# Kernel optimization log

Hardware: AMD Instinct MI355X
Metric: run time of the kernel (lower is better)

Reference implementation:

```python
import jax, jax.numpy as jnp
import numpy as np

N_NODES = 50000
N_EDGES = 800000
IN_CH = 64
OC = 16  # out_channels


def setup_inputs() -> dict:
    key = jax.random.key(0)
    ks = jax.random.split(key, 16)
    x = jax.random.normal(ks[0], (N_NODES, IN_CH), dtype=jnp.float32)
    edge_index = jax.random.randint(ks[1], (2, N_EDGES), 0, N_NODES, dtype=jnp.int64)

    def lin(k, fan_in, fan_out):
        s = 1.0 / np.sqrt(fan_in)
        return jax.random.uniform(k, (fan_in, fan_out), jnp.float32, -s, s)

    d1, d2 = 16 * OC, 8 * OC  # 256, 128
    return {
        "x": x,
        "W1_rel": lin(ks[2], IN_CH, d1), "b1": jnp.zeros((d1,), jnp.float32), "W1_root": lin(ks[3], IN_CH, d1),
        "W2_rel": lin(ks[4], d1, d2), "b2": jnp.zeros((d2,), jnp.float32), "W2_root": lin(ks[5], d1, d2),
        "Wmu_rel": lin(ks[6], d2, OC), "bmu": jnp.zeros((OC,), jnp.float32), "Wmu_root": lin(ks[7], d2, OC),
        "Wls_rel": lin(ks[8], d2, OC), "bls": jnp.zeros((OC,), jnp.float32), "Wls_root": lin(ks[9], d2, OC),
        "edge_index": edge_index,
    }


def _graph_conv(x, src, dst, deg_inv, W_rel, b, W_root):
    # PyG GraphConv(aggr='mean'): out = lin_rel(mean_{j in N(i)} x_j) + lin_root(x_i)
    msg_sum = jax.ops.segment_sum(x[src], dst, num_segments=x.shape[0])  # [N, d]
    agg = msg_sum * deg_inv[:, None]
    return agg @ W_rel + b + x @ W_root


def reference(x, W1_rel, b1, W1_root, W2_rel, b2, W2_root,
              Wmu_rel, bmu, Wmu_root, Wls_rel, bls, Wls_root, edge_index):
    src, dst = edge_index[0], edge_index[1]
    deg = jax.ops.segment_sum(jnp.ones_like(dst, dtype=x.dtype), dst, num_segments=x.shape[0])
    deg_inv = jnp.where(deg > 0, 1.0 / jnp.maximum(deg, 1.0), 0.0)

    h = jax.nn.relu(_graph_conv(x, src, dst, deg_inv, W1_rel, b1, W1_root))
    h = jax.nn.relu(_graph_conv(h, src, dst, deg_inv, W2_rel, b2, W2_root))
    mu = _graph_conv(h, src, dst, deg_inv, Wmu_rel, bmu, Wmu_root)
    logstd = _graph_conv(h, src, dst, deg_inv, Wls_rel, bls, Wls_root)
    return (mu, logstd)
```

## Files before the change

kernel.cpp:

```cpp
#include <hip/hip_runtime.h>
#include <hip/hip_fp8.h>

#define N_NODES 50000
#define N_EDGES 800000
#define NBUCK 196
#define PBLK 391
#define CAP 5120

typedef unsigned short ushort_t;
typedef unsigned char uchar_t;
typedef short short8 __attribute__((ext_vector_type(8)));
typedef float floatx4 __attribute__((ext_vector_type(4)));

__device__ __forceinline__ float bf2f(ushort_t u) {
    unsigned v = ((unsigned)u) << 16;
    return __builtin_bit_cast(float, v);
}
__device__ __forceinline__ ushort_t f2bf(float f) {
    unsigned u = __builtin_bit_cast(unsigned, f);
    unsigned r = (u + 0x7FFFu + ((u >> 16) & 1u)) >> 16;
    return (ushort_t)r;
}
__device__ __forceinline__ uchar_t f2fp8(float f) {
    __hip_fp8_e4m3 t(f);
    return (uchar_t)t.__x;
}
__device__ __forceinline__ float fp82f(uchar_t u) {
    __hip_fp8_e4m3 t;
    t.__x = (__hip_fp8_storage_t)u;
    return (float)t;
}
__device__ __forceinline__ float4 ld4(const float* p) { return *(const float4*)p; }

__global__ __launch_bounds__(256) void prep_kernel(
    const float* __restrict__ x,
    const float* __restrict__ W1_rel, const float* __restrict__ W1_root,
    const float* __restrict__ W2_rel, const float* __restrict__ W2_root,
    const float* __restrict__ Wmu_rel, const float* __restrict__ Wls_rel,
    const float* __restrict__ Wmu_root, const float* __restrict__ Wls_root,
    ushort_t* __restrict__ xb, uchar_t* __restrict__ xq,
    ushort_t* __restrict__ B1t, ushort_t* __restrict__ B2t, ushort_t* __restrict__ B3t,
    int* __restrict__ bcursor) {
    int idx = blockIdx.x * blockDim.x + threadIdx.x;
    if (idx < 400000) {
        int n = idx >> 3, c = (idx & 7) * 8;
        float4 v0 = ld4(x + (size_t)n * 64 + c);
        float4 v1 = ld4(x + (size_t)n * 64 + c + 4);
        float vv[8] = {v0.x, v0.y, v0.z, v0.w, v1.x, v1.y, v1.z, v1.w};
        short8 o;
        unsigned q0 = 0, q1 = 0;
        #pragma unroll
        for (int i = 0; i < 4; ++i) {
            o[i] = f2bf(vv[i]);
            o[4 + i] = f2bf(vv[4 + i]);
            q0 |= ((unsigned)f2fp8(vv[i])) << (8 * i);
            q1 |= ((unsigned)f2fp8(vv[4 + i])) << (8 * i);
        }
        *(short8*)(xb + (size_t)n * 64 + c) = o;
        uint2 q = {q0, q1};
        *(uint2*)(xq + (size_t)n * 64 + c) = q;
    } else if (idx < 506496) {
        int j = idx - 400000;
        if (j < 32768) {
            int n = j >> 7, k = j & 127;
            float v = (k < 64) ? W1_rel[k * 256 + n] : W1_root[(k - 64) * 256 + n];
            B1t[j] = f2bf(v);
        } else if (j < 98304) {
            int jj = j - 32768;
            int n = jj >> 8, k = jj & 255;
            float v = (n < 128) ? W2_rel[k * 128 + n] : W2_root[k * 128 + (n - 128)];
            B2t[jj] = f2bf(v);
        } else {
            int jj = j - 98304;
            int n = jj >> 7, k = jj & 127;
            const float* W = (n < 16) ? Wmu_rel : (n < 32) ? Wls_rel : (n < 48) ? Wmu_root : Wls_root;
            B3t[jj] = f2bf(W[k * 16 + (n & 15)]);
        }
    } else if (idx < 506496 + NBUCK) {
        int b = idx - 506496;
        bcursor[b] = b * CAP;
    }
}

__global__ __launch_bounds__(256) void partition_kernel(
    const int* __restrict__ src, const int* __restrict__ dst,
    int* __restrict__ bcursor, unsigned* __restrict__ pairbuf) {
    __shared__ int h[NBUCK];
    __shared__ int cur[NBUCK];
    const int tid = threadIdx.x;
    for (int i = tid; i < NBUCK; i += 256) h[i] = 0;
    __syncthreads();
    const int base = blockIdx.x * 2048;
    int d[8];
    #pragma unroll
    for (int j = 0; j < 8; ++j) {
        int e = base + j * 256 + tid;
        if (e < N_EDGES) { d[j] = dst[e]; atomicAdd(&h[d[j] >> 8], 1); }
        else d[j] = -1;
    }
    __syncthreads();
    for (int i = tid; i < NBUCK; i += 256) {
        int c = h[i];
        cur[i] = c ? atomicAdd(&bcursor[i], c) : 0;
    }
    __syncthreads();
    #pragma unroll
    for (int j = 0; j < 8; ++j) {
        int e = base + j * 256 + tid;
        if (e < N_EDGES) {
            int dd = d[j];
            int slot = atomicAdd(&cur[dd >> 8], 1);
            pairbuf[slot] = (unsigned)src[e] | ((unsigned)(dd & 255) << 16);
        }
    }
}

__global__ __launch_bounds__(256) void fill_bucket_kernel(
    const unsigned* __restrict__ pairbuf, const int* __restrict__ bcursor,
    int* __restrict__ row_beg, int* __restrict__ row_end,
    float* __restrict__ dinv, ushort_t* __restrict__ eidx) {
    __shared__ int h[256];
    __shared__ int sm[256];
    __shared__ int cur[256];
    const int b = blockIdx.x, tid = threadIdx.x;
    const int beg = b * CAP, end = bcursor[b];
    h[tid] = 0;
    __syncthreads();
    for (int i = beg + tid; i < end; i += 256)
        atomicAdd(&h[pairbuf[i] >> 16], 1);
    __syncthreads();
    int c = h[tid];
    sm[tid] = c;
    __syncthreads();
    #pragma unroll
    for (int off = 1; off < 256; off <<= 1) {
        int t = (tid >= off) ? sm[tid - off] : 0;
        __syncthreads();
        sm[tid] += t;
        __syncthreads();
    }
    int exc = beg + sm[tid] - c;
    int node = b * 256 + tid;
    if (node < N_NODES) {
        row_beg[node] = exc;
        row_end[node] = exc + c;
        dinv[node] = c > 0 ? 1.0f / (float)c : 0.0f;
    }
    cur[tid] = exc;
    __syncthreads();
    for (int i = beg + tid; i < end; i += 256) {
        unsigned v = pairbuf[i];
        int slot = atomicAdd(&cur[v >> 16], 1);
        eidx[slot] = (ushort_t)(v & 0xFFFFu);
    }
}

__global__ __launch_bounds__(256) void g1gemm12(
    const ushort_t* __restrict__ xb, const uchar_t* __restrict__ xq,
    const int* __restrict__ row_beg, const int* __restrict__ row_end,
    const ushort_t* __restrict__ eidx, const float* __restrict__ dinv,
    const ushort_t* __restrict__ B1t, const float* __restrict__ b1,
    const ushort_t* __restrict__ B2t,
    uchar_t* __restrict__ t2, ushort_t* __restrict__ r2) {
    constexpr int K1 = 128, K2 = 256;
    constexpr int AKP = 72;
    constexpr int HKP = 264;
    constexpr int BKP = 264;
    __shared__ ushort_t As[64 * AKP];
    __shared__ ushort_t Hs[64 * HKP];
    __shared__ ushort_t Bs[64 * BKP];
    const int tid = threadIdx.x;
    const int rowbase = blockIdx.x * 64;

    {
        const int nl = tid >> 2, lane = tid & 3;
        const int node = rowbase + nl;
        int beg = 0, end = 0;
        float d = 0.0f;
        if (node < N_NODES) { beg = row_beg[node]; end = row_end[node]; d = dinv[node]; }
        float a0[16] = {}, a1[16] = {};
        int j = beg;
        for (; j + 1 < end; j += 2) {
            uint4 v0 = *(const uint4*)(xq + (size_t)eidx[j] * 64 + lane * 16);
            uint4 v1 = *(const uint4*)(xq + (size_t)eidx[j + 1] * 64 + lane * 16);
            #pragma unroll
            for (int i = 0; i < 4; ++i) {
                a0[i]      += fp82f((uchar_t)(v0.x >> (8 * i)));
                a0[4 + i]  += fp82f((uchar_t)(v0.y >> (8 * i)));
                a0[8 + i]  += fp82f((uchar_t)(v0.z >> (8 * i)));
                a0[12 + i] += fp82f((uchar_t)(v0.w >> (8 * i)));
                a1[i]      += fp82f((uchar_t)(v1.x >> (8 * i)));
                a1[4 + i]  += fp82f((uchar_t)(v1.y >> (8 * i)));
                a1[8 + i]  += fp82f((uchar_t)(v1.z >> (8 * i)));
                a1[12 + i] += fp82f((uchar_t)(v1.w >> (8 * i)));
            }
        }
        if (j < end) {
            uint4 v0 = *(const uint4*)(xq + (size_t)eidx[j] * 64 + lane * 16);
            #pragma unroll
            for (int i = 0; i < 4; ++i) {
                a0[i]      += fp82f((uchar_t)(v0.x >> (8 * i)));
                a0[4 + i]  += fp82f((uchar_t)(v0.y >> (8 * i)));
                a0[8 + i]  += fp82f((uchar_t)(v0.z >> (8 * i)));
                a0[12 + i] += fp82f((uchar_t)(v0.w >> (8 * i)));
            }
        }
        short8 o0, o1;
        #pragma unroll
        for (int i = 0; i < 8; ++i) {
            o0[i] = f2bf((a0[i] + a1[i]) * d);
            o1[i] = f2bf((a0[8 + i] + a1[8 + i]) * d);
        }
        *(short8*)(As + nl * AKP + lane * 16) = o0;
        *(short8*)(As + nl * AKP + lane * 16 + 8) = o1;
    }
    __syncthreads();

    const int w = tid >> 6, lane64 = tid & 63;
    const int ln = lane64 & 15, quad = lane64 >> 4;
    const int rwl = w * 16 + ln;
    int r = rowbase + rwl;
    if (r > N_NODES - 1) r = N_NODES - 1;

    short8 a[4];
    a[0] = *(const short8*)(As + rwl * AKP + quad * 8);
    a[1] = *(const short8*)(As + rwl * AKP + 32 + quad * 8);
    a[2] = *(const short8*)(xb + (size_t)r * 64 + quad * 8);
    a[3] = *(const short8*)(xb + (size_t)r * 64 + 32 + quad * 8);
    for (int ny = 0; ny < 4; ++ny) {
        __syncthreads();
        for (int i = tid; i < 64 * 16; i += 256) {
            int row = i >> 4, off = (i & 15) * 8;
            *(short8*)(Bs + row * BKP + off) = *(const short8*)(B1t + (size_t)(ny * 64 + row) * K1 + off);
        }
        __syncthreads();
        floatx4 acc[4] = {};
        #pragma unroll
        for (int f = 0; f < 4; ++f) {
            const ushort_t* bp = Bs + (f * 16 + ln) * BKP + quad * 8;
            #pragma unroll
            for (int s = 0; s < 4; ++s) {
                short8 b = *(const short8*)(bp + s * 32);
                acc[f] = __builtin_amdgcn_mfma_f32_16x16x32_bf16(a[s], b, acc[f], 0, 0, 0);
            }
        }
        #pragma unroll
        for (int f = 0; f < 4; ++f) {
            int n = ny * 64 + f * 16 + ln;
            float bias = b1[n];
            #pragma unroll
            for (int g = 0; g < 4; ++g) {
                int rr = w * 16 + quad * 4 + g;
                Hs[rr * HKP + n] = f2bf(fmaxf(acc[f][g] + bias, 0.0f));
            }
        }
    }
    __syncthreads();

    short8 a2[8];
    #pragma unroll
    for (int s = 0; s < 8; ++s)
        a2[s] = *(const short8*)(Hs + rwl * HKP + s * 32 + quad * 8);
    for (int ny = 0; ny < 4; ++ny) {
        __syncthreads();
        for (int i = tid; i < 64 * 32; i += 256) {
            int row = i >> 5, off = (i & 31) * 8;
            *(short8*)(Bs + row * BKP + off) = *(const short8*)(B2t + (size_t)(ny * 64 + row) * K2 + off);
        }
        __syncthreads();
        floatx4 acc[4] = {};
        #pragma unroll
        for (int f = 0; f < 4; ++f) {
            const ushort_t* bp = Bs + (f * 16 + ln) * BKP + quad * 8;
            #pragma unroll
            for (int s = 0; s < 8; ++s) {
                short8 b = *(const short8*)(bp + s * 32);
                acc[f] = __builtin_amdgcn_mfma_f32_16x16x32_bf16(a2[s], b, acc[f], 0, 0, 0);
            }
        }
        #pragma unroll
        for (int f = 0; f < 4; ++f) {
            int n = ny * 64 + f * 16 + ln;
            #pragma unroll
            for (int g = 0; g < 4; ++g) {
                int rr = rowbase + w * 16 + quad * 4 + g;
                if (rr >= N_NODES) continue;
                float v = acc[f][g];
                if (n < 128) t2[(size_t)rr * 128 + n] = f2fp8(v);
                else r2[(size_t)rr * 128 + (n - 128)] = f2bf(v);
            }
        }
    }
}

__global__ __launch_bounds__(256) void g2g3_kernel(
    const uchar_t* __restrict__ t2, const ushort_t* __restrict__ r2,
    const int* __restrict__ row_beg, const int* __restrict__ row_end,
    const ushort_t* __restrict__ eidx, const float* __restrict__ dinv,
    const float* __restrict__ b2, const ushort_t* __restrict__ B3t,
    ushort_t* __restrict__ tml, float* __restrict__ rml) {
    constexpr int KP = 136;
    __shared__ ushort_t As[16 * KP];
    const int tid = threadIdx.x;
    const int nb = blockIdx.x * 16;
    {
        const int nl = tid >> 4, lane = tid & 15;
        const int node = nb + nl;
        const int beg = row_beg[node], end = row_end[node];
        float a0[8] = {}, a1[8] = {}, a2[8] = {}, a3[8] = {};
        int j = beg;
        for (; j + 3 < end; j += 4) {
            uint2 v0 = *(const uint2*)(t2 + (size_t)eidx[j] * 128 + lane * 8);
            uint2 v1 = *(const uint2*)(t2 + (size_t)eidx[j + 1] * 128 + lane * 8);
            uint2 v2 = *(const uint2*)(t2 + (size_t)eidx[j + 2] * 128 + lane * 8);
            uint2 v3 = *(const uint2*)(t2 + (size_t)eidx[j + 3] * 128 + lane * 8);
            #pragma unroll
            for (int i = 0; i < 4; ++i) {
                a0[i]     += fp82f((uchar_t)(v0.x >> (8 * i)));
                a0[4 + i] += fp82f((uchar_t)(v0.y >> (8 * i)));
                a1[i]     += fp82f((uchar_t)(v1.x >> (8 * i)));
                a1[4 + i] += fp82f((uchar_t)(v1.y >> (8 * i)));
                a2[i]     += fp82f((uchar_t)(v2.x >> (8 * i)));
                a2[4 + i] += fp82f((uchar_t)(v2.y >> (8 * i)));
                a3[i]     += fp82f((uchar_t)(v3.x >> (8 * i)));
                a3[4 + i] += fp82f((uchar_t)(v3.y >> (8 * i)));
            }
        }
        for (; j < end; ++j) {
            uint2 v0 = *(const uint2*)(t2 + (size_t)eidx[j] * 128 + lane * 8);
            #pragma unroll
            for (int i = 0; i < 4; ++i) {
                a0[i]     += fp82f((uchar_t)(v0.x >> (8 * i)));
                a0[4 + i] += fp82f((uchar_t)(v0.y >> (8 * i)));
            }
        }
        float d = dinv[node];
        short8 rv = *(const short8*)(r2 + (size_t)node * 128 + lane * 8);
        float4 ba = ld4(b2 + lane * 8), bb = ld4(b2 + lane * 8 + 4);
        float bc[8] = {ba.x, ba.y, ba.z, ba.w, bb.x, bb.y, bb.z, bb.w};
        short8 o;
        #pragma unroll
        for (int i = 0; i < 8; ++i)
            o[i] = f2bf(fmaxf(((a0[i] + a1[i]) + (a2[i] + a3[i])) * d + bf2f((ushort_t)rv[i]) + bc[i], 0.0f));
        *(short8*)(As + nl * KP + lane * 8) = o;
    }
    __syncthreads();
    const int w = tid >> 6, lane64 = tid & 63;
    const int ln = lane64 & 15, quad = lane64 >> 4;
    short8 a[4];
    #pragma unroll
    for (int s = 0; s < 4; ++s)
        a[s] = *(const short8*)(As + ln * KP + s * 32 + quad * 8);
    floatx4 acc = {};
    const ushort_t* bp = B3t + (size_t)(w * 16 + ln) * 128 + quad * 8;
    #pragma unroll
    for (int s = 0; s < 4; ++s) {
        short8 b = *(const short8*)(bp + s * 32);
        acc = __builtin_amdgcn_mfma_f32_16x16x32_bf16(a[s], b, acc, 0, 0, 0);
    }
    const int r0 = nb + quad * 4;
    const int ncol = w * 16 + ln;
    #pragma unroll
    for (int g = 0; g < 4; ++g) {
        int rr = r0 + g;
        float v = acc[g];
        if (ncol < 32) tml[(size_t)rr * 32 + ncol] = f2bf(v);
        else rml[(size_t)rr * 32 + (ncol - 32)] = v;
    }
}

__global__ __launch_bounds__(256) void gather3_kernel(
    const ushort_t* __restrict__ tml, const float* __restrict__ rml,
    const int* __restrict__ row_beg, const int* __restrict__ row_end,
    const ushort_t* __restrict__ eidx, const float* __restrict__ dinv,
    const float* __restrict__ bmu, const float* __restrict__ bls,
    float* __restrict__ out) {
    const int lane = threadIdx.x & 3;
    const int nl = threadIdx.x >> 2;
    const int n = blockIdx.x * 64 + nl;
    if (n >= N_NODES) return;
    const int beg = row_beg[n], end = row_end[n];
    float a0[8] = {}, a1[8] = {}, a2[8] = {}, a3[8] = {};
    int j = beg;
    for (; j + 3 < end; j += 4) {
        short8 v0 = *(const short8*)(tml + (size_t)eidx[j] * 32 + lane * 8);
        short8 v1 = *(const short8*)(tml + (size_t)eidx[j + 1] * 32 + lane * 8);
        short8 v2 = *(const short8*)(tml + (size_t)eidx[j + 2] * 32 + lane * 8);
        short8 v3 = *(const short8*)(tml + (size_t)eidx[j + 3] * 32 + lane * 8);
        #pragma unroll
        for (int i = 0; i < 8; ++i) {
            a0[i] += bf2f((ushort_t)v0[i]); a1[i] += bf2f((ushort_t)v1[i]);
            a2[i] += bf2f((ushort_t)v2[i]); a3[i] += bf2f((ushort_t)v3[i]);
        }
    }
    for (; j < end; ++j) {
        short8 v0 = *(const short8*)(tml + (size_t)eidx[j] * 32 + lane * 8);
        #pragma unroll
        for (int i = 0; i < 8; ++i) a0[i] += bf2f((ushort_t)v0[i]);
    }
    float d = dinv[n];
    const float* bias = (lane < 2) ? (bmu + lane * 8) : (bls + (lane - 2) * 8);
    float4 ra = ld4(rml + (size_t)n * 32 + lane * 8);
    float4 rb = ld4(rml + (size_t)n * 32 + lane * 8 + 4);
    float4 ba = ld4(bias);
    float4 bb = ld4(bias + 4);
    float rr[8] = {ra.x, ra.y, ra.z, ra.w, rb.x, rb.y, rb.z, rb.w};
    float bc[8] = {ba.x, ba.y, ba.z, ba.w, bb.x, bb.y, bb.z, bb.w};
    float res[8];
    #pragma unroll
    for (int i = 0; i < 8; ++i) res[i] = ((a0[i] + a1[i]) + (a2[i] + a3[i])) * d + rr[i] + bc[i];
    float* base = (lane < 2) ? (out + (size_t)n * 16 + lane * 8)
                             : (out + 800000u + (size_t)n * 16 + (lane - 2) * 8);
    *(float4*)(base) = make_float4(res[0], res[1], res[2], res[3]);
    *(float4*)(base + 4) = make_float4(res[4], res[5], res[6], res[7]);
}

extern "C" void kernel_launch(void* const* d_in, const int* in_sizes, int n_in,
                              void* d_out, int out_size, void* d_ws, size_t ws_size,
                              hipStream_t stream) {
    const float* x       = (const float*)d_in[0];
    const float* W1_rel  = (const float*)d_in[1];
    const float* b1      = (const float*)d_in[2];
    const float* W1_root = (const float*)d_in[3];
    const float* W2_rel  = (const float*)d_in[4];
    const float* b2      = (const float*)d_in[5];
    const float* W2_root = (const float*)d_in[6];
    const float* Wmu_rel = (const float*)d_in[7];
    const float* bmu     = (const float*)d_in[8];
    const float* Wmu_root= (const float*)d_in[9];
    const float* Wls_rel = (const float*)d_in[10];
    const float* bls     = (const float*)d_in[11];
    const float* Wls_root= (const float*)d_in[12];
    const int*   ei      = (const int*)d_in[13];
    const int* src = ei;
    const int* dst = ei + N_EDGES;

    int*      bcursor = (int*)d_ws;
    int*      row_beg = bcursor + 256;
    int*      row_end = row_beg + 50048;
    unsigned* pairbuf = (unsigned*)(row_end + 50048);
    ushort_t* eidx    = (ushort_t*)(pairbuf + 1003520);
    float*    dinv    = (float*)(eidx + 1003520);
    ushort_t* xb   = (ushort_t*)(dinv + 50000);
    uchar_t*  xq   = (uchar_t*)(xb + 3200000);
    uchar_t*  t2   = xq + 3200000;
    ushort_t* r2   = (ushort_t*)(t2 + 6400000);
    ushort_t* tml  = r2 + 6400000;
    ushort_t* B1t  = tml + 1600000;
    ushort_t* B2t  = B1t + 32768;
    ushort_t* B3t  = B2t + 65536;
    float* rml     = (float*)(B3t + 8192);
    float* out     = (float*)d_out;

    prep_kernel<<<1980, 256, 0, stream>>>(x, W1_rel, W1_root, W2_rel, W2_root,
                                          Wmu_rel, Wls_rel, Wmu_root, Wls_root,
                                          xb, xq, B1t, B2t, B3t, bcursor);
    partition_kernel<<<PBLK, 256, 0, stream>>>(src, dst, bcursor, pairbuf);
    fill_bucket_kernel<<<NBUCK, 256, 0, stream>>>(pairbuf, bcursor, row_beg, row_end, dinv, eidx);

    g1gemm12<<<782, 256, 0, stream>>>(xb, xq, row_beg, row_end, eidx, dinv,
                                      B1t, b1, B2t, t2, r2);

    g2g3_kernel<<<3125, 256, 0, stream>>>(t2, r2, row_beg, row_end, eidx, dinv, b2, B3t, tml, rml);

    gather3_kernel<<<782, 256, 0, stream>>>(tml, rml, row_beg, row_end, eidx, dinv, bmu, bls, out);
}
```

Baseline: 220.6 us.

## Read GEMM weights directly from global memory and drop the shared B tile

Removes the shared-memory B staging buffer in the fused gather+GEMM kernel, so the MFMA loops load weight fragments straight from global memory (L2/L1-resident) with no block barriers per tile. Cutting LDS use and adding a launch-bounds occupancy hint of 3 blocks aims for higher occupancy. The edge gather loop is also unrolled to four neighbours per iteration for more memory-level parallelism. The risk is more global and cache traffic for the weights, plus register pressure from the occupancy cap.

Measured after the change: 265.1 us. +20.2%, slower.

```diff
diff --git a/kernel.cpp b/kernel.cpp
--- a/kernel.cpp
+++ b/kernel.cpp
@@ -31,6 +31,16 @@
     return (float)t;
 }
 __device__ __forceinline__ float4 ld4(const float* p) { return *(const float4*)p; }
+
+__device__ __forceinline__ void acc16(float* a, uint4 v) {
+    unsigned ws[4] = {v.x, v.y, v.z, v.w};
+    #pragma unroll
+    for (int wi = 0; wi < 4; ++wi) {
+        #pragma unroll
+        for (int i = 0; i < 4; ++i)
+            a[wi * 4 + i] += fp82f((uchar_t)(ws[wi] >> (8 * i)));
+    }
+}
 
 __global__ __launch_bounds__(256) void prep_kernel(
     const float* __restrict__ x,
@@ -155,7 +165,7 @@
     }
 }
 
-__global__ __launch_bounds__(256) void g1gemm12(
+__global__ __launch_bounds__(256, 3) void g1gemm12(
     const ushort_t* __restrict__ xb, const uchar_t* __restrict__ xq,
     const int* __restrict__ row_beg, const int* __restrict__ row_end,
     const ushort_t* __restrict__ eidx, const float* __restrict__ dinv,
@@ -165,10 +175,8 @@
     constexpr int K1 = 128, K2 = 256;
     constexpr int AKP = 72;
     constexpr int HKP = 264;
-    constexpr int BKP = 264;
     __shared__ ushort_t As[64 * AKP];
     __shared__ ushort_t Hs[64 * HKP];
-    __shared__ ushort_t Bs[64 * BKP];
     const int tid = threadIdx.x;
     const int rowbase = blockIdx.x * 64;
 
@@ -180,30 +188,16 @@
         if (node < N_NODES) { beg = row_beg[node]; end = row_end[node]; d = dinv[node]; }
         float a0[16] = {}, a1[16] = {};
         int j = beg;
-        for (; j + 1 < end; j += 2) {
+        for (; j + 3 < end; j += 4) {
             uint4 v0 = *(const uint4*)(xq + (size_t)eidx[j] * 64 + lane * 16);
             uint4 v1 = *(const uint4*)(xq + (size_t)eidx[j + 1] * 64 + lane * 16);
-            #pragma unroll
-            for (int i = 0; i < 4; ++i) {
-                a0[i]      += fp82f((uchar_t)(v0.x >> (8 * i)));
-                a0[4 + i]  += fp82f((uchar_t)(v0.y >> (8 * i)));
-                a0[8 + i]  += fp82f((uchar_t)(v0.z >> (8 * i)));
-                a0[12 + i] += fp82f((uchar_t)(v0.w >> (8 * i)));
-                a1[i]      += fp82f((uchar_t)(v1.x >> (8 * i)));
-                a1[4 + i]  += fp82f((uchar_t)(v1.y >> (8 * i)));
-                a1[8 + i]  += fp82f((uchar_t)(v1.z >> (8 * i)));
-                a1[12 + i] += fp82f((uchar_t)(v1.w >> (8 * i)));
-            }
-        }
-        if (j < end) {
+            uint4 v2 = *(const uint4*)(xq + (size_t)eidx[j + 2] * 64 + lane * 16);
+            uint4 v3 = *(const uint4*)(xq + (size_t)eidx[j + 3] * 64 + lane * 16);
+            acc16(a0, v0); acc16(a1, v1); acc16(a0, v2); acc16(a1, v3);
+        }
+        for (; j < end; ++j) {
             uint4 v0 = *(const uint4*)(xq + (size_t)eidx[j] * 64 + lane * 16);
-            #pragma unroll
-            for (int i = 0; i < 4; ++i) {
-                a0[i]      += fp82f((uchar_t)(v0.x >> (8 * i)));
-                a0[4 + i]  += fp82f((uchar_t)(v0.y >> (8 * i)));
-                a0[8 + i]  += fp82f((uchar_t)(v0.z >> (8 * i)));
-                a0[12 + i] += fp82f((uchar_t)(v0.w >> (8 * i)));
-            }
+            acc16(a0, v0);
         }
         short8 o0, o1;
         #pragma unroll
@@ -228,16 +222,10 @@
     a[2] = *(const short8*)(xb + (size_t)r * 64 + quad * 8);
     a[3] = *(const short8*)(xb + (size_t)r * 64 + 32 + quad * 8);
     for (int ny = 0; ny < 4; ++ny) {
-        __syncthreads();
-        for (int i = tid; i < 64 * 16; i += 256) {
-            int row = i >> 4, off = (i & 15) * 8;
-            *(short8*)(Bs + row * BKP + off) = *(const short8*)(B1t + (size_t)(ny * 64 + row) * K1 + off);
-        }
-        __syncthreads();
         floatx4 acc[4] = {};
         #pragma unroll
         for (int f = 0; f < 4; ++f) {
-            const ushort_t* bp = Bs + (f * 16 + ln) * BKP + quad * 8;
+            const ushort_t* bp = B1t + (size_t)(ny * 64 + f * 16 + ln) * K1 + quad * 8;
             #pragma unroll
             for (int s = 0; s < 4; ++s) {
                 short8 b = *(const short8*)(bp + s * 32);
@@ -262,16 +250,10 @@
     for (int s = 0; s < 8; ++s)
         a2[s] = *(const short8*)(Hs + rwl * HKP + s * 32 + quad * 8);
     for (int ny = 0; ny < 4; ++ny) {
-        __syncthreads();
-        for (int i = tid; i < 64 * 32; i += 256) {
-            int row = i >> 5, off = (i & 31) * 8;
-            *(short8*)(Bs + row * BKP + off) = *(const short8*)(B2t + (size_t)(ny * 64 + row) * K2 + off);
-        }
-        __syncthreads();
         floatx4 acc[4] = {};
         #pragma unroll
         for (int f = 0; f < 4; ++f) {
-            const ushort_t* bp = Bs + (f * 16 + ln) * BKP + quad * 8;
+            const ushort_t* bp = B2t + (size_t)(ny * 64 + f * 16 + ln) * K2 + quad * 8;
             #pragma unroll
             for (int s = 0; s < 8; ++s) {
                 short8 b = *(const short8*)(bp + s * 32);
```
